# Kernel tuning notes

Measured on AMD Instinct MI355X. Metric: run time of the kernel, lower is better.

The kernel has to match this reference:

```python
import jax, jax.numpy as jnp
import numpy as np

N_EMBD = 768
HIDDEN = 4 * N_EMBD
N_EXPERTS = 8
TOP_K = 2


def setup_inputs() -> dict:
    key = jax.random.key(0)
    ks = jax.random.split(key, 4)
    B, T, C, E, H = 4, 2048, N_EMBD, N_EXPERTS, HIDDEN
    x = jax.random.normal(ks[0], (B, T, C), dtype=jnp.float32)
    gate_w = jax.random.normal(ks[1], (E, C), dtype=jnp.float32) * 0.02
    gate_b = jnp.zeros((E,), dtype=jnp.float32)
    w_fc = jax.random.normal(ks[2], (E, H, C), dtype=jnp.float32) * 0.02
    b_fc = jnp.zeros((E, H), dtype=jnp.float32)
    w_proj = jax.random.normal(ks[3], (E, C, H), dtype=jnp.float32) * 0.02
    b_proj = jnp.zeros((E, C), dtype=jnp.float32)
    return {"x": x, "gate_w": gate_w, "gate_b": gate_b, "w_fc": w_fc,
            "b_fc": b_fc, "w_proj": w_proj, "b_proj": b_proj}


def reference(x, gate_w, gate_b, w_fc, b_fc, w_proj, b_proj):
    B, T, C = x.shape
    E = gate_b.shape[0]
    xf = x.reshape(-1, C)  # [N, C]
    # gating: Linear(C -> E), top-k, softmax over the k selected scores
    scores = xf @ gate_w.T + gate_b                      # [N, E]
    top_s, top_i = jax.lax.top_k(scores, TOP_K)          # [N, K]
    gates = jax.nn.softmax(top_s, axis=-1)               # [N, K]
    # combine weight per (token, expert): sum_k gate[t,k] * 1[top_i[t,k]==e]
    comb = jnp.sum(jax.nn.one_hot(top_i, E, dtype=xf.dtype) * gates[..., None], axis=1)  # [N, E]
    out = jnp.zeros_like(xf)
    for j in range(E):  # loop over fixed small expert count
        h = jax.nn.gelu(xf @ w_fc[j].T + b_fc[j], approximate=True)  # [N, H]
        y = h @ w_proj[j].T + b_proj[j]                              # [N, C]
        out = out + comb[:, j:j + 1] * y
    return out.reshape(B, T, C)
```

## Files before the change

kernel.cpp:

```cpp
#include <hip/hip_runtime.h>
#include <cmath>

#define N_TOK 8192
#define C_DIM 768
#define H_DIM 3072
#define NEXP  8
#define PADCAP 18432

typedef short short8 __attribute__((ext_vector_type(8)));
typedef float f32x4  __attribute__((ext_vector_type(4)));

__device__ __forceinline__ unsigned short f2b(float f) {
  unsigned int u = __float_as_uint(f);
  u += 0x7fffu + ((u >> 16) & 1u);
  return (unsigned short)(u >> 16);
}
__device__ __forceinline__ float b2f(unsigned short u) {
  return __uint_as_float((unsigned int)u << 16);
}
__device__ __forceinline__ void gll(const char* g, char* l) {
  __builtin_amdgcn_global_load_lds((const __attribute__((address_space(1))) void*)g,
                                   (__attribute__((address_space(3))) void*)l, 16, 0, 0);
}

__global__ __launch_bounds__(256) void gate_kernel(
    const float* __restrict__ x, const float* __restrict__ gw,
    const float* __restrict__ gb, int* __restrict__ counts,
    int* __restrict__ tok_e, int* __restrict__ tok_r, float* __restrict__ tok_w) {
  __shared__ float gwl[NEXP * C_DIM];
  __shared__ double red[256][NEXP];
  int tid = threadIdx.x;
  const float4* gw4 = (const float4*)gw;
  float4* gl4 = (float4*)gwl;
  for (int i = tid; i < NEXP * C_DIM / 4; i += 256) gl4[i] = gw4[i];
  __syncthreads();
  int tl = tid & 63;
  int kc = tid >> 6;
  int t = blockIdx.x * 64 + tl;
  double acc[NEXP];
#pragma unroll
  for (int e = 0; e < NEXP; e++) acc[e] = 0.0;
  const float* xr = x + (size_t)t * C_DIM;
  for (int k = kc * 192; k < kc * 192 + 192; k++) {
    double xv = (double)xr[k];
#pragma unroll
    for (int e = 0; e < NEXP; e++) acc[e] += xv * (double)gwl[e * C_DIM + k];
  }
#pragma unroll
  for (int e = 0; e < NEXP; e++) red[tid][e] = acc[e];
  __syncthreads();
  if (tid < 64) {
    double s[NEXP];
#pragma unroll
    for (int e = 0; e < NEXP; e++)
      s[e] = (double)gb[e] + red[tid][e] + red[tid + 64][e] + red[tid + 128][e] + red[tid + 192][e];
    double best = s[0], sec = -1e300; int bi = 0, si = -1;
#pragma unroll
    for (int e = 1; e < NEXP; e++) {
      if (s[e] > best)      { sec = best; si = bi; best = s[e]; bi = e; }
      else if (s[e] > sec)  { sec = s[e]; si = e; }
    }
    double ex = exp(sec - best);
    double den = 1.0 + ex;
    tok_e[2 * t] = bi;  tok_e[2 * t + 1] = si;
    tok_w[2 * t] = (float)(1.0 / den);  tok_w[2 * t + 1] = (float)(ex / den);
    tok_r[2 * t]     = atomicAdd(&counts[bi], 1);
    tok_r[2 * t + 1] = atomicAdd(&counts[si], 1);
  }
}

__global__ void offsets_kernel(const int* __restrict__ counts, int* __restrict__ po) {
  if (threadIdx.x == 0 && blockIdx.x == 0) {
    int s = 0;
    for (int e = 0; e < NEXP; e++) { po[e] = s; s += (counts[e] + 255) & ~255; }
    po[NEXP] = s;
  }
}

__global__ __launch_bounds__(256) void scatter_kernel(
    const int* __restrict__ tok_e, const int* __restrict__ tok_r,
    const float* __restrict__ tok_w, const int* __restrict__ po,
    int* __restrict__ perm_t, float* __restrict__ perm_w,
    int* __restrict__ tok_pos) {
  int t = blockIdx.x * 256 + threadIdx.x;
#pragma unroll
  for (int k = 0; k < 2; k++) {
    int e = tok_e[2 * t + k];
    int pos = po[e] + tok_r[2 * t + k];
    perm_t[pos] = t;
    perm_w[pos] = tok_w[2 * t + k];
    tok_pos[2 * t + k] = pos;
  }
}

__global__ __launch_bounds__(256) void gather_kernel(
    const float* __restrict__ x, const int* __restrict__ po,
    const int* __restrict__ perm_t, unsigned short* __restrict__ xg) {
  int row = blockIdx.x * 4 + (threadIdx.x >> 6);
  if (row >= po[NEXP]) return;
  int l = threadIdx.x & 63;
  int t = perm_t[row];
  const float4* src = (const float4*)(x + (size_t)t * C_DIM);
  ushort4* dst = (ushort4*)(xg + (size_t)row * C_DIM);
#pragma unroll
  for (int j = 0; j < 3; j++) {
    float4 v = src[l + j * 64];
    ushort4 o; o.x = f2b(v.x); o.y = f2b(v.y); o.z = f2b(v.z); o.w = f2b(v.w);
    dst[l + j * 64] = o;
  }
}

__global__ __launch_bounds__(256) void wconv_kernel(
    const float* __restrict__ src, unsigned short* __restrict__ dst, int n4) {
  int stride = gridDim.x * blockDim.x;
  for (int i = blockIdx.x * blockDim.x + threadIdx.x; i < n4; i += stride) {
    float4 v = ((const float4*)src)[i];
    ushort4 o; o.x = f2b(v.x); o.y = f2b(v.y); o.z = f2b(v.z); o.w = f2b(v.w);
    ((ushort4*)dst)[i] = o;
  }
}

__device__ __forceinline__ void gemm8p(
    const char* __restrict__ Ab, size_t ldaB,
    const char* __restrict__ Bb, size_t ldbB, int ktiles,
    char* lds, int tid, f32x4 acc[8][4]) {
  const int w = tid >> 6, l = tid & 63;
  const int wr = w >> 2, wc = w & 3;
  const int lr = l & 15, kc = l >> 4;
  const int sw = (lr >> 1) & 7;
  const int s0 = ((kc ^ sw) << 4);
  const int s1 = s0 ^ 64;
  const int arow = ((wr << 7) + lr) << 7;
  const int brow = 32768 + (((wc << 6) + lr) << 7);
  const int rl0 = tid >> 3;
  const int cg0 = (tid & 7) ^ ((rl0 >> 1) & 7);
  const size_t oA0 = (size_t)rl0 * ldaB + (cg0 << 4);
  const size_t oA1 = oA0 + (ldaB << 6);
  const size_t oB0 = (size_t)rl0 * ldbB + (cg0 << 4);
  const size_t oB1 = oB0 + (ldbB << 6);
  const int wb = w << 10;

#define SA(b, h, kt) do { \
    const char* s_ = Ab + (size_t)(h) * 128 * ldaB + (size_t)(kt) * 128; \
    gll(s_ + oA0, lds + (b) * 65536 + (h) * 16384 + wb); \
    gll(s_ + oA1, lds + (b) * 65536 + (h) * 16384 + 8192 + wb); } while (0)
#define SB(b, h, kt) do { \
    const char* s_ = Bb + (size_t)(h) * 128 * ldbB + (size_t)(kt) * 128; \
    gll(s_ + oB0, lds + (b) * 65536 + 32768 + (h) * 16384 + wb); \
    gll(s_ + oB1, lds + (b) * 65536 + 32768 + (h) * 16384 + 8192 + wb); } while (0)
#define BAR() asm volatile("s_barrier" ::: "memory")
#define RDA(B, mb) do { \
    for (int mi = 0; mi < 4; mi++) { \
      af[mi][0] = *(const short8*)(lds + (B) + arow + ((mb) + mi) * 2048 + s0); \
      af[mi][1] = *(const short8*)(lds + (B) + arow + ((mb) + mi) * 2048 + s1); } } while (0)
#define RDB(B, nb) do { \
    for (int ni = 0; ni < 2; ni++) { \
      bf[(nb) + ni][0] = *(const short8*)(lds + (B) + brow + ((nb) + ni) * 2048 + s0); \
      bf[(nb) + ni][1] = *(const short8*)(lds + (B) + brow + ((nb) + ni) * 2048 + s1); } } while (0)
#define MM(mb, nb) do { \
    __builtin_amdgcn_s_setprio(1); \
    for (int mi = 0; mi < 4; mi++) \
      for (int ni = 0; ni < 2; ni++) \
        for (int kk = 0; kk < 2; kk++) \
          acc[(mb) + mi][(nb) + ni] = __builtin_amdgcn_mfma_f32_16x16x32_bf16( \
              af[mi][kk], bf[(nb) + ni][kk], acc[(mb) + mi][(nb) + ni], 0, 0, 0); \
    __builtin_amdgcn_s_setprio(0); } while (0)

  short8 af[4][2], bf[4][2];
  SB(0, 0, 0); SB(0, 1, 0); SA(0, 0, 0); SA(0, 1, 0);
  SB(1, 0, 1); SB(1, 1, 1);
  asm volatile("s_waitcnt vmcnt(4)" ::: "memory");
  BAR();
  const int iters = ktiles >> 1;
#pragma unroll 1
  for (int i = 0; i < iters; i++) {
    const int t1 = 2 * i + 1, t2 = 2 * i + 2, t3 = 2 * i + 3;
    const bool nl = (i + 1 < iters);
    RDA(0, 0); RDB(0, 0);
    SA(1, 0, t1);
    BAR(); MM(0, 0); BAR();
    RDB(0, 2);
    SA(1, 1, t1);
    BAR(); MM(0, 2); BAR();
    RDA(0, 4);
    if (nl) SB(0, 0, t2);
    BAR(); MM(4, 2); BAR();
    if (nl) SB(0, 1, t2);
    BAR(); MM(4, 0);
    if (nl) asm volatile("s_waitcnt vmcnt(4)" ::: "memory");
    else    asm volatile("s_waitcnt vmcnt(0)" ::: "memory");
    BAR();
    RDA(65536, 0); RDB(65536, 0);
    if (nl) SA(0, 0, t2);
    BAR(); MM(0, 0); BAR();
    RDB(65536, 2);
    if (nl) SA(0, 1, t2);
    BAR(); MM(0, 2); BAR();
    RDA(65536, 4);
    if (nl) SB(1, 0, t3);
    BAR(); MM(4, 2); BAR();
    if (nl) SB(1, 1, t3);
    BAR(); MM(4, 0);
    if (nl) {
      asm volatile("s_waitcnt vmcnt(4)" ::: "memory");
      BAR();
    }
  }
#undef SA
#undef SB
#undef BAR
#undef RDA
#undef RDB
#undef MM
}

__global__ __launch_bounds__(512, 2) void fc1_kernel(
    const unsigned short* __restrict__ xg, const unsigned short* __restrict__ wfcb,
    const float* __restrict__ bfc, const int* __restrict__ po,
    unsigned short* __restrict__ h) {
  __shared__ char lds[131072];
  int bid = blockIdx.x;
  int r8 = bid & 7, g8 = bid >> 3;
  int col = g8 % 12;
  int Sp  = g8 / 12;
  int y   = r8 * 9 + Sp;
  int row0 = y * 256;
  if (row0 >= po[NEXP]) return;
  int e = 0;
#pragma unroll
  for (int i = 1; i < NEXP; i++) if (row0 >= po[i]) e = i;
  int n0 = col * 256;
  int tid = threadIdx.x;
  f32x4 acc[8][4];
#pragma unroll
  for (int mi = 0; mi < 8; mi++)
#pragma unroll
    for (int ni = 0; ni < 4; ni++) acc[mi][ni] = (f32x4){0.f, 0.f, 0.f, 0.f};
  gemm8p((const char*)(xg + (size_t)row0 * C_DIM), (size_t)C_DIM * 2,
         (const char*)(wfcb + (size_t)e * H_DIM * C_DIM + (size_t)n0 * C_DIM),
         (size_t)C_DIM * 2, C_DIM / 64, lds, tid, acc);
  int w = tid >> 6, l = tid & 63;
  int wr = w >> 2, wc = w & 3, lr = l & 15, q = l >> 4;
  const float* bias = bfc + (size_t)e * H_DIM;
#pragma unroll
  for (int ni = 0; ni < 4; ni++) {
    int colw = n0 + wc * 64 + ni * 16 + lr;
    float bv = bias[colw];
#pragma unroll
    for (int mi = 0; mi < 8; mi++) {
#pragma unroll
      for (int r = 0; r < 4; r++) {
        int row = row0 + wr * 128 + mi * 16 + q * 4 + r;
        float v = acc[mi][ni][r] + bv;
        float z = v * fmaf(0.0356774081f, v * v, 0.7978845608f);
        float ex = __builtin_amdgcn_exp2f(-2.8853900818f * z);
        float g = v * __builtin_amdgcn_rcpf(1.0f + ex);
        h[(size_t)row * H_DIM + colw] = f2b(g);
      }
    }
  }
}

__global__ __launch_bounds__(512, 2) void fc2_kernel(
    const unsigned short* __restrict__ h, const unsigned short* __restrict__ wpjb,
    const float* __restrict__ bproj, const int* __restrict__ po,
    const float* __restrict__ perm_w, unsigned short* __restrict__ part) {
  __shared__ char lds[131072];
  int bid = blockIdx.x;
  int r8 = bid & 7, g8 = bid >> 3;
  int col = g8 % 3;
  int Sp  = g8 / 3;
  int y   = r8 * 9 + Sp;
  int row0 = y * 256;
  if (row0 >= po[NEXP]) return;
  int e = 0;
#pragma unroll
  for (int i = 1; i < NEXP; i++) if (row0 >= po[i]) e = i;
  int n0 = col * 256;
  int tid = threadIdx.x;
  f32x4 acc[8][4];
#pragma unroll
  for (int mi = 0; mi < 8; mi++)
#pragma unroll
    for (int ni = 0; ni < 4; ni++) acc[mi][ni] = (f32x4){0.f, 0.f, 0.f, 0.f};
  gemm8p((const char*)(h + (size_t)row0 * H_DIM), (size_t)H_DIM * 2,
         (const char*)(wpjb + (size_t)e * C_DIM * H_DIM + (size_t)n0 * H_DIM),
         (size_t)H_DIM * 2, H_DIM / 64, lds, tid, acc);
  int w = tid >> 6, l = tid & 63;
  int wr = w >> 2, wc = w & 3, lr = l & 15, q = l >> 4;
  const float* bias = bproj + (size_t)e * C_DIM;
#pragma unroll
  for (int mi = 0; mi < 8; mi++) {
#pragma unroll
    for (int r = 0; r < 4; r++) {
      int pos = row0 + wr * 128 + mi * 16 + q * 4 + r;
      float wgt = perm_w[pos];
#pragma unroll
      for (int ni = 0; ni < 4; ni++) {
        int colw = n0 + wc * 64 + ni * 16 + lr;
        float v = acc[mi][ni][r] + bias[colw];
        part[(size_t)pos * C_DIM + colw] = f2b(v * wgt);
      }
    }
  }
}

__global__ __launch_bounds__(256) void combine_kernel(
    const unsigned short* __restrict__ part, const int* __restrict__ tok_pos,
    float* __restrict__ out) {
  const int NC4 = C_DIM / 4;
  int idx = blockIdx.x * 256 + threadIdx.x;
  int t = idx / NC4, c4 = idx - t * NC4;
  int p0 = tok_pos[2 * t], p1 = tok_pos[2 * t + 1];
  ushort4 v0 = *(const ushort4*)(part + (size_t)p0 * C_DIM + c4 * 4);
  ushort4 v1 = *(const ushort4*)(part + (size_t)p1 * C_DIM + c4 * 4);
  float4 o;
  o.x = b2f(v0.x) + b2f(v1.x);
  o.y = b2f(v0.y) + b2f(v1.y);
  o.z = b2f(v0.z) + b2f(v1.z);
  o.w = b2f(v0.w) + b2f(v1.w);
  ((float4*)out)[idx] = o;
}

extern "C" void kernel_launch(void* const* d_in, const int* in_sizes, int n_in,
                              void* d_out, int out_size, void* d_ws, size_t ws_size,
                              hipStream_t stream) {
  const float* x     = (const float*)d_in[0];
  const float* gw    = (const float*)d_in[1];
  const float* gb    = (const float*)d_in[2];
  const float* wfc   = (const float*)d_in[3];
  const float* bfc   = (const float*)d_in[4];
  const float* wproj = (const float*)d_in[5];
  const float* bproj = (const float*)d_in[6];
  float* out = (float*)d_out;
  char* ws = (char*)d_ws;

  int*   counts  = (int*)(ws + 0);
  int*   po      = (int*)(ws + 64);
  int*   tok_e   = (int*)(ws + 256);
  int*   tok_r   = (int*)(ws + 65792);
  float* tok_w   = (float*)(ws + 131328);
  int*   tok_pos = (int*)(ws + 196864);
  int*   perm_t  = (int*)(ws + 262400);
  float* perm_w  = (float*)(ws + 336128);
  const size_t ROUT_END = 409856;
  unsigned short* wfcb = (unsigned short*)(ws + 409856);
  unsigned short* wpjb = (unsigned short*)(ws + 409856);
  unsigned short* xg   = (unsigned short*)(ws + 38158592);
  unsigned short* part = (unsigned short*)(ws + 38158592);
  unsigned short* hbuf = (unsigned short*)(ws + 66470144);

  hipMemsetAsync(ws, 0, ROUT_END, stream);

  const int WN4 = NEXP * H_DIM * C_DIM / 4;
  gate_kernel<<<N_TOK / 64, 256, 0, stream>>>(x, gw, gb, counts, tok_e, tok_r, tok_w);
  offsets_kernel<<<1, 64, 0, stream>>>(counts, po);
  scatter_kernel<<<N_TOK / 256, 256, 0, stream>>>(tok_e, tok_r, tok_w, po, perm_t, perm_w, tok_pos);
  gather_kernel<<<PADCAP / 4, 256, 0, stream>>>(x, po, perm_t, xg);
  wconv_kernel<<<2048, 256, 0, stream>>>(wfc, wfcb, WN4);
  fc1_kernel<<<8 * 9 * 12, 512, 0, stream>>>(xg, wfcb, bfc, po, hbuf);
  wconv_kernel<<<2048, 256, 0, stream>>>(wproj, wpjb, WN4);
  fc2_kernel<<<8 * 9 * 3, 512, 0, stream>>>(hbuf, wpjb, bproj, po, perm_w, part);
  combine_kernel<<<N_TOK * (C_DIM / 4) / 256, 256, 0, stream>>>(part, tok_pos, out);
}
```

Before: 505.7 us.

## Rewrite fc1 with 128x128 tiles, double-buffered LDS, and staged coalesced output

Replaces the 256x256-tile fc1 GEMM with a new 128x128-tile core that uses a simple double-buffered global_load_lds pipeline. This raises the block count and allows four blocks per CU instead of two. The GELU epilogue now writes bf16 results into padded LDS and then stores them to global memory as 16-byte vectors, replacing the scattered 2-byte stores. The smaller tiles give more parallelism and better tail balance across padded expert segments, at the cost of lower operand reuse per block and more global traffic.

After: 498.4 us. About the same (-1.4%).

```diff
diff --git a/kernel.cpp b/kernel.cpp
--- a/kernel.cpp
+++ b/kernel.cpp
@@ -8,6 +8,7 @@
 #define PADCAP 18432
 
 typedef short short8 __attribute__((ext_vector_type(8)));
+typedef unsigned short ushort8 __attribute__((ext_vector_type(8)));
 typedef float f32x4  __attribute__((ext_vector_type(4)));
 
 __device__ __forceinline__ unsigned short f2b(float f) {
@@ -117,6 +118,118 @@
     float4 v = ((const float4*)src)[i];
     ushort4 o; o.x = f2b(v.x); o.y = f2b(v.y); o.z = f2b(v.z); o.w = f2b(v.w);
     ((ushort4*)dst)[i] = o;
+  }
+}
+
+__device__ __forceinline__ void gemm_core512(
+    const unsigned short* A, int lda, const unsigned short* B, int ldb, int K,
+    char* lds, int tid, f32x4 acc[4][2]) {
+  const int w = tid >> 6, l = tid & 63;
+  const int wr = w >> 2, wc = w & 3;
+  const int rowa = wr * 64 + (l & 15);
+  const int rowb = wc * 32 + (l & 15);
+  const int kc = l >> 4;
+  const int sa0 = (kc ^ ((rowa >> 1) & 7)) * 16;
+  const int sb0 = (kc ^ ((rowb >> 1) & 7)) * 16;
+  const int r0 = tid >> 3,          cg0 = (tid & 7) ^ ((r0 >> 1) & 7);
+  const int r1 = (512 + tid) >> 3,  cg1 = ((512 + tid) & 7) ^ ((r1 >> 1) & 7);
+  const char* gA0 = (const char*)(A + (size_t)r0 * lda) + cg0 * 16;
+  const char* gA1 = (const char*)(A + (size_t)r1 * lda) + cg1 * 16;
+  const char* gB0 = (const char*)(B + (size_t)r0 * ldb) + cg0 * 16;
+  const char* gB1 = (const char*)(B + (size_t)r1 * ldb) + cg1 * 16;
+  const int wb = w * 1024;
+  const int iters = K >> 6;
+  gll(gA0, lds + wb);
+  gll(gA1, lds + 8192 + wb);
+  gll(gB0, lds + 16384 + wb);
+  gll(gB1, lds + 24576 + wb);
+#pragma unroll 1
+  for (int kt = 0; kt < iters; kt++) {
+    __syncthreads();
+    if (kt + 1 < iters) {
+      size_t kb = (size_t)(kt + 1) * 128;
+      char* nb = lds + ((kt + 1) & 1) * 32768;
+      gll(gA0 + kb, nb + wb);
+      gll(gA1 + kb, nb + 8192 + wb);
+      gll(gB0 + kb, nb + 16384 + wb);
+      gll(gB1 + kb, nb + 24576 + wb);
+    }
+    char* bb = lds + (kt & 1) * 32768;
+#pragma unroll
+    for (int s = 0; s < 2; s++) {
+      const int sxa = sa0 ^ (s << 6);
+      const int sxb = sb0 ^ (s << 6);
+      short8 af[4], bf2[2];
+#pragma unroll
+      for (int mi = 0; mi < 4; mi++)
+        af[mi] = *(const short8*)(bb + (rowa + mi * 16) * 128 + sxa);
+#pragma unroll
+      for (int ni = 0; ni < 2; ni++)
+        bf2[ni] = *(const short8*)(bb + 16384 + (rowb + ni * 16) * 128 + sxb);
+#pragma unroll
+      for (int mi = 0; mi < 4; mi++)
+#pragma unroll
+        for (int ni = 0; ni < 2; ni++)
+          acc[mi][ni] = __builtin_amdgcn_mfma_f32_16x16x32_bf16(af[mi], bf2[ni], acc[mi][ni], 0, 0, 0);
+    }
+  }
+}
+
+__global__ __launch_bounds__(512, 4) void fc1_kernel(
+    const unsigned short* __restrict__ xg, const unsigned short* __restrict__ wfcb,
+    const float* __restrict__ bfc, const int* __restrict__ po,
+    unsigned short* __restrict__ h) {
+  __shared__ char lds[65536];
+  int bid = blockIdx.x;
+  int r8 = bid & 7, g8 = bid >> 3;
+  int col = g8 % 24;
+  int Sp  = g8 / 24;
+  int y   = r8 * 18 + Sp;
+  int row0 = y * 128;
+  if (row0 >= po[NEXP]) return;
+  int e = 0;
+#pragma unroll
+  for (int i = 1; i < NEXP; i++) if (row0 >= po[i]) e = i;
+  int n0 = col * 128;
+  int tid = threadIdx.x;
+  f32x4 acc[4][2];
+#pragma unroll
+  for (int mi = 0; mi < 4; mi++)
+#pragma unroll
+    for (int ni = 0; ni < 2; ni++) acc[mi][ni] = (f32x4){0.f, 0.f, 0.f, 0.f};
+  gemm_core512(xg + (size_t)row0 * C_DIM, C_DIM,
+               wfcb + (size_t)e * H_DIM * C_DIM + (size_t)n0 * C_DIM, C_DIM, C_DIM,
+               lds, tid, acc);
+  int w = tid >> 6, l = tid & 63;
+  int wr = w >> 2, wc = w & 3, q = l >> 4, lr = l & 15;
+  const float* bias = bfc + (size_t)e * H_DIM;
+  __syncthreads();
+  unsigned short* lout = (unsigned short*)lds;
+  const int LST = 136;
+#pragma unroll
+  for (int ni = 0; ni < 2; ni++) {
+    int lcol = wc * 32 + ni * 16 + lr;
+    float bv = bias[n0 + lcol];
+#pragma unroll
+    for (int mi = 0; mi < 4; mi++) {
+#pragma unroll
+      for (int r = 0; r < 4; r++) {
+        int lrow = wr * 64 + mi * 16 + q * 4 + r;
+        float v = acc[mi][ni][r] + bv;
+        float z = v * fmaf(0.0356774081f, v * v, 0.7978845608f);
+        float ex = __builtin_amdgcn_exp2f(-2.8853900818f * z);
+        float g = v * __builtin_amdgcn_rcpf(1.0f + ex);
+        lout[lrow * LST + lcol] = f2b(g);
+      }
+    }
+  }
+  __syncthreads();
+#pragma unroll
+  for (int p = 0; p < 4; p++) {
+    int idx = p * 512 + tid;
+    int row = idx >> 4, c8 = idx & 15;
+    ushort8 v = *(const ushort8*)(lout + row * LST + c8 * 8);
+    *(ushort8*)(h + (size_t)(row0 + row) * H_DIM + n0 + c8 * 8) = v;
   }
 }
 
@@ -214,53 +327,6 @@
 #undef MM
 }
 
-__global__ __launch_bounds__(512, 2) void fc1_kernel(
-    const unsigned short* __restrict__ xg, const unsigned short* __restrict__ wfcb,
-    const float* __restrict__ bfc, const int* __restrict__ po,
-    unsigned short* __restrict__ h) {
-  __shared__ char lds[131072];
-  int bid = blockIdx.x;
-  int r8 = bid & 7, g8 = bid >> 3;
-  int col = g8 % 12;
-  int Sp  = g8 / 12;
-  int y   = r8 * 9 + Sp;
-  int row0 = y * 256;
-  if (row0 >= po[NEXP]) return;
-  int e = 0;
-#pragma unroll
-  for (int i = 1; i < NEXP; i++) if (row0 >= po[i]) e = i;
-  int n0 = col * 256;
-  int tid = threadIdx.x;
-  f32x4 acc[8][4];
-#pragma unroll
-  for (int mi = 0; mi < 8; mi++)
-#pragma unroll
-    for (int ni = 0; ni < 4; ni++) acc[mi][ni] = (f32x4){0.f, 0.f, 0.f, 0.f};
-  gemm8p((const char*)(xg + (size_t)row0 * C_DIM), (size_t)C_DIM * 2,
-         (const char*)(wfcb + (size_t)e * H_DIM * C_DIM + (size_t)n0 * C_DIM),
-         (size_t)C_DIM * 2, C_DIM / 64, lds, tid, acc);
-  int w = tid >> 6, l = tid & 63;
-  int wr = w >> 2, wc = w & 3, lr = l & 15, q = l >> 4;
-  const float* bias = bfc + (size_t)e * H_DIM;
-#pragma unroll
-  for (int ni = 0; ni < 4; ni++) {
-    int colw = n0 + wc * 64 + ni * 16 + lr;
-    float bv = bias[colw];
-#pragma unroll
-    for (int mi = 0; mi < 8; mi++) {
-#pragma unroll
-      for (int r = 0; r < 4; r++) {
-        int row = row0 + wr * 128 + mi * 16 + q * 4 + r;
-        float v = acc[mi][ni][r] + bv;
-        float z = v * fmaf(0.0356774081f, v * v, 0.7978845608f);
-        float ex = __builtin_amdgcn_exp2f(-2.8853900818f * z);
-        float g = v * __builtin_amdgcn_rcpf(1.0f + ex);
-        h[(size_t)row * H_DIM + colw] = f2b(g);
-      }
-    }
-  }
-}
-
 __global__ __launch_bounds__(512, 2) void fc2_kernel(
     const unsigned short* __restrict__ h, const unsigned short* __restrict__ wpjb,
     const float* __restrict__ bproj, const int* __restrict__ po,
@@ -358,7 +424,7 @@
   scatter_kernel<<<N_TOK / 256, 256, 0, stream>>>(tok_e, tok_r, tok_w, po, perm_t, perm_w, tok_pos);
   gather_kernel<<<PADCAP / 4, 256, 0, stream>>>(x, po, perm_t, xg);
   wconv_kernel<<<2048, 256, 0, stream>>>(wfc, wfcb, WN4);
-  fc1_kernel<<<8 * 9 * 12, 512, 0, stream>>>(xg, wfcb, bfc, po, hbuf);
+  fc1_kernel<<<8 * 18 * 24, 512, 0, stream>>>(xg, wfcb, bfc, po, hbuf);
   wconv_kernel<<<2048, 256, 0, stream>>>(wproj, wpjb, WN4);
   fc2_kernel<<<8 * 9 * 3, 512, 0, stream>>>(hbuf, wpjb, bproj, po, perm_w, part);
   combine_kernel<<<N_TOK * (C_DIM / 4) / 256, 256, 0, stream>>>(part, tok_pos, out);
```
